# Performance work log

Measured on AMD Instinct MI355X. Metric: run time of the kernel, lower is better.

Reference implementation:

```python
import jax, jax.numpy as jnp
import numpy as np

N_HEADS = 8
N_POINTS = 4


def setup_inputs() -> dict:
    key = jax.random.key(0)
    ks = jax.random.split(key, 10)
    B, Q, D = 8, 2048, 256
    Hh, Ww = 100, 100
    s = 0.02  # init scale for weights
    return {
        "query": jax.random.normal(ks[0], (B, Q, D), jnp.float32),
        "reference_points": jax.random.uniform(ks[1], (B, Q, 2), jnp.float32),
        "input_flatten": jax.random.normal(ks[2], (B, Hh * Ww, D), jnp.float32),
        "h": Hh,
        "w": Ww,
        "W_off": jax.random.normal(ks[3], (D, N_HEADS * N_POINTS * 2), jnp.float32) * s,
        "b_off": jnp.zeros((N_HEADS * N_POINTS * 2,), jnp.float32),
        "W_attn": jax.random.normal(ks[4], (D, N_HEADS * N_POINTS), jnp.float32) * s,
        "b_attn": jnp.zeros((N_HEADS * N_POINTS,), jnp.float32),
        "W_val": jax.random.normal(ks[5], (D, D), jnp.float32) * s,
        "b_val": jnp.zeros((D,), jnp.float32),
        "W_out": jax.random.normal(ks[6], (D, D), jnp.float32) * s,
        "b_out": jnp.zeros((D,), jnp.float32),
    }


def _gather(values_heads, idx):
    # values_heads: [B, HW, H, Dh]; idx: [B, Q, H, P] -> [B, Q, H, P, Dh]
    B, HW, H, Dh = values_heads.shape
    b = jnp.arange(B)[:, None, None, None]
    hh = jnp.arange(H)[None, None, :, None]
    return values_heads[b, idx, hh, :]


def reference(query, reference_points, input_flatten, h, w,
              W_off, b_off, W_attn, b_attn, W_val, b_val, W_out, b_out):
    B, Q, D = query.shape
    HW = input_flatten.shape[1]
    nH, nP = N_HEADS, N_POINTS
    Dh = D // nH

    offsets = (query @ W_off + b_off).reshape(B, Q, nH, nP, 2)
    weights = jax.nn.softmax((query @ W_attn + b_attn).reshape(B, Q, nH, nP), axis=-1)
    values_heads = (input_flatten @ W_val + b_val).reshape(B, HW, nH, Dh)

    # sampling locations in [0,1], then to pixel coords
    loc = jnp.clip(reference_points[:, :, None, None, :] + offsets, 0.0, 1.0)
    sx = loc[..., 0] * (w - 1)  # [B,Q,H,P]
    sy = loc[..., 1] * (h - 1)

    x0 = jnp.clip(jnp.floor(sx).astype(jnp.int32), 0, w - 1)
    y0 = jnp.clip(jnp.floor(sy).astype(jnp.int32), 0, h - 1)
    x1 = jnp.clip(x0 + 1, 0, w - 1)
    y1 = jnp.clip(y0 + 1, 0, h - 1)

    wx1 = sx - x0.astype(sx.dtype)
    wx0 = 1.0 - wx1
    wy1 = sy - y0.astype(sy.dtype)
    wy0 = 1.0 - wy1

    g00 = _gather(values_heads, y0 * w + x0)
    g01 = _gather(values_heads, y1 * w + x0)
    g10 = _gather(values_heads, y0 * w + x1)
    g11 = _gather(values_heads, y1 * w + x1)

    # bilinear blend: [B,Q,H,P,Dh]
    result = (g00 * (wx0 * wy0)[..., None] + g01 * (wx0 * wy1)[..., None]
              + g10 * (wx1 * wy0)[..., None] + g11 * (wx1 * wy1)[..., None])

    out = jnp.sum(result * weights[..., None], axis=3)  # [B,Q,H,Dh]
    out = out.reshape(B, Q, D)
    return out @ W_out + b_out
```

## Files before the change

kernel.cpp:

```cpp
#include <hip/hip_runtime.h>
#include <hip/hip_bf16.h>
#include <cstdint>

#define NHEADS 8
#define NPOINTS 4

typedef __bf16 bf16x8 __attribute__((ext_vector_type(8)));
typedef float f32x4 __attribute__((ext_vector_type(4)));

#define AS1 __attribute__((address_space(1)))
#define AS3 __attribute__((address_space(3)))

__device__ __forceinline__ ushort f2bf_rn(float x) {
  union { float f; uint32_t u; } c; c.f = x;
  uint32_t r = c.u + 0x7fffu + ((c.u >> 16) & 1u);
  return (ushort)(r >> 16);
}
__device__ __forceinline__ float bf2f(ushort h) {
  union { uint32_t u; float f; } c; c.u = ((uint32_t)h) << 16; return c.f;
}
__device__ __forceinline__ uint pack2(ushort a, ushort b) {
  return (uint)a | ((uint)b << 16);
}

__device__ __forceinline__ int fr(int row) { return (row >> 1) & 3; }
__device__ __forceinline__ int aidx(int row, int gpos) { return row * 32 + gpos * 8; }

__device__ __forceinline__ int gidx8(int row, int g0) {
  return row * 64 + ((g0 ^ (row & 7)) << 3);
}

template<int TM, bool CBF16, bool ABF16>
__device__ __forceinline__ void gemm_core(
    ushort* smem, int bid,
    const void* __restrict__ Ain,
    const ushort* __restrict__ Bprep,
    const float* __restrict__ bias, void* __restrict__ Cout,
    int K)
{
  constexpr int MT = TM / 16;
  constexpr int AH = TM * 32;
  constexpr int BH = 8192;
  const int tid  = threadIdx.x;
  const int lane = tid & 63, wave = tid >> 6;
  const int wn   = wave * 64;
  const int lrow = lane & 15, lgrp = lane >> 4;
  const long brow = (long)bid * TM;
  const int NT = K >> 5;

  const float*  Af = (const float*)Ain;
  const ushort* A16 = (const ushort*)Ain;

  f32x4 acc[MT][4] = {};

  int arow, as_;
  if constexpr (TM == 64) { arow = tid >> 2; as_ = tid & 3; }
  else                    { arow = tid >> 3; as_ = tid & 7; }

  ushort* Acur = smem;
  ushort* Anxt = smem + AH;
  ushort* Bcur = smem + 2 * AH;
  ushort* Bnxt = smem + 2 * AH + BH;

#pragma unroll
  for (int i = 0; i < 4; ++i)
    __builtin_amdgcn_global_load_lds(
        (const AS1 void*)(Bprep + wave * 2048 + (lane + 64 * i) * 8),
        (AS3 void*)(Bcur + wave * 2048 + (lane + 64 * i) * 8), 16, 0, 0);
  if constexpr (ABF16) {
    uint2 av = *(const uint2*)&A16[(size_t)(brow + arow) * K + as_ * 4];
    const int g = as_ >> 1, half = (as_ & 1) * 4;
    *(uint2*)&Acur[aidx(arow, g ^ fr(arow)) + half] = av;
  } else if constexpr (TM == 64) {
    const float* ap = &Af[(size_t)(brow + arow) * K] + as_ * 8;
    float4 a0 = *(const float4*)ap, a1 = *(const float4*)(ap + 4);
    const float v[8] = {a0.x, a0.y, a0.z, a0.w, a1.x, a1.y, a1.z, a1.w};
    ushort h[8];
#pragma unroll
    for (int j = 0; j < 8; ++j) h[j] = f2bf_rn(v[j]);
    uint4 hv = {pack2(h[0],h[1]), pack2(h[2],h[3]), pack2(h[4],h[5]), pack2(h[6],h[7])};
    *(uint4*)&Acur[aidx(arow, as_ ^ fr(arow))] = hv;
  } else {
    const int g = as_ >> 1, half = (as_ & 1) * 4;
    float4 a0 = *(const float4*)&Af[(size_t)(brow + arow) * K + g * 8 + half];
    ushort h[4] = {f2bf_rn(a0.x), f2bf_rn(a0.y), f2bf_rn(a0.z), f2bf_rn(a0.w)};
    uint2 hv = {pack2(h[0],h[1]), pack2(h[2],h[3])};
    *(uint2*)&Acur[aidx(arow, g ^ fr(arow)) + half] = hv;
  }
  __syncthreads();

  for (int t = 0; t < NT; ++t) {
    const bool more = (t + 1 < NT);

    if (more) {
#pragma unroll
      for (int i = 0; i < 4; ++i)
        __builtin_amdgcn_global_load_lds(
            (const AS1 void*)(Bprep + (size_t)(t + 1) * BH + wave * 2048 + (lane + 64 * i) * 8),
            (AS3 void*)(Bnxt + wave * 2048 + (lane + 64 * i) * 8), 16, 0, 0);
    }

    float4 a0 = {}, a1 = {};
    uint2 au = {};
    if (more) {
      if constexpr (ABF16) {
        au = *(const uint2*)&A16[(size_t)(brow + arow) * K + (t + 1) * 32 + as_ * 4];
      } else if constexpr (TM == 64) {
        const float* ap = &Af[(size_t)(brow + arow) * K] + (t + 1) * 32 + as_ * 8;
        a0 = *(const float4*)ap;
        a1 = *(const float4*)(ap + 4);
      } else {
        const int g = as_ >> 1, half = (as_ & 1) * 4;
        a0 = *(const float4*)&Af[(size_t)(brow + arow) * K + (t + 1) * 32 + g * 8 + half];
      }
    }

    bf16x8 ah[MT];
#pragma unroll
    for (int mt = 0; mt < MT; ++mt) {
      const int r = mt * 16 + lrow;
      ah[mt] = *(const bf16x8*)&Acur[aidx(r, lgrp ^ fr(r))];
    }
#pragma unroll
    for (int nt = 0; nt < 4; ++nt) {
      const int r = wn + nt * 16 + lrow;
      const bf16x8 b = *(const bf16x8*)&Bcur[aidx(r, lgrp ^ fr(r))];
#pragma unroll
      for (int mt = 0; mt < MT; ++mt)
        acc[mt][nt] = __builtin_amdgcn_mfma_f32_16x16x32_bf16(ah[mt], b, acc[mt][nt], 0, 0, 0);
    }

    if (more) {
      if constexpr (ABF16) {
        const int g = as_ >> 1, half = (as_ & 1) * 4;
        *(uint2*)&Anxt[aidx(arow, g ^ fr(arow)) + half] = au;
      } else if constexpr (TM == 64) {
        const float v[8] = {a0.x, a0.y, a0.z, a0.w, a1.x, a1.y, a1.z, a1.w};
        ushort h[8];
#pragma unroll
        for (int j = 0; j < 8; ++j) h[j] = f2bf_rn(v[j]);
        uint4 hv = {pack2(h[0],h[1]), pack2(h[2],h[3]), pack2(h[4],h[5]), pack2(h[6],h[7])};
        *(uint4*)&Anxt[aidx(arow, as_ ^ fr(arow))] = hv;
      } else {
        const int g = as_ >> 1, half = (as_ & 1) * 4;
        ushort h[4] = {f2bf_rn(a0.x), f2bf_rn(a0.y), f2bf_rn(a0.z), f2bf_rn(a0.w)};
        uint2 hv = {pack2(h[0],h[1]), pack2(h[2],h[3])};
        *(uint2*)&Anxt[aidx(arow, g ^ fr(arow)) + half] = hv;
      }
    }

    __syncthreads();
    ushort* tp;
    tp = Acur; Acur = Anxt; Anxt = tp;
    tp = Bcur; Bcur = Bnxt; Bnxt = tp;
  }

  float bb[4];
#pragma unroll
  for (int nt = 0; nt < 4; ++nt) bb[nt] = bias[wn + nt * 16 + lrow];

  if constexpr (CBF16) {
    ushort* Cb = (ushort*)Cout;
    ushort* ctu = smem;
#pragma unroll
    for (int h = 0; h < TM / 32; ++h) {
      __syncthreads();
#pragma unroll
      for (int m2 = 0; m2 < 2; ++m2) {
        const int mt = h * 2 + m2;
        const int lr0 = m2 * 16 + lgrp * 4;
#pragma unroll
        for (int nt = 0; nt < 4; ++nt) {
          const int col = wn + nt * 16 + lrow;
#pragma unroll
          for (int j = 0; j < 4; ++j)
            ctu[(lr0 + j) * 264 + col] = f2bf_rn(acc[mt][nt][j] + bb[nt]);
        }
      }
      __syncthreads();
#pragma unroll
      for (int i = 0; i < 4; ++i) {
        const int idx = i * 256 + tid, r = idx >> 5, c16 = (idx & 31) * 8;
        *(uint4*)&Cb[(size_t)(brow + h * 32 + r) * 256 + c16] =
            *(const uint4*)&ctu[r * 264 + c16];
      }
    }
  } else {
    float* C = (float*)Cout;
    float* ctile = (float*)smem;
#pragma unroll
    for (int h = 0; h < MT; ++h) {
      __syncthreads();
#pragma unroll
      for (int nt = 0; nt < 4; ++nt) {
        const int col = wn + nt * 16 + lrow;
#pragma unroll
        for (int j = 0; j < 4; ++j)
          ctile[(lgrp * 4 + j) * 260 + col] = acc[h][nt][j] + bb[nt];
      }
      __syncthreads();
#pragma unroll
      for (int i = 0; i < 4; ++i) {
        const int idx = i * 256 + tid, r = idx >> 6, c4 = (idx & 63) << 2;
        *(float4*)&C[(size_t)(brow + h * 16 + r) * 256 + c4] =
            *(const float4*)&ctile[r * 260 + c4];
      }
    }
  }
}

__device__ __forceinline__ void proj_core(
    ushort* smem, int bid,
    const float* __restrict__ query,
    const ushort* __restrict__ Bprep,
    const float* __restrict__ b_off, const float* __restrict__ b_attn,
    float* __restrict__ pobuf)
{
  constexpr int AH = 32 * 64;
  constexpr int BH = 8192;
  const int tid  = threadIdx.x;
  const int lane = tid & 63, wave = tid >> 6;
  const int wm   = (wave >> 1) * 16;
  const int wn   = (wave & 1) * 64;
  const int lrow = lane & 15, lgrp = lane >> 4;
  const long brow = (long)bid * 32;

  f32x4 acc[4] = {};

  const int arow = tid >> 3, as_ = tid & 7;
  const float* Abase = &query[(size_t)(brow + arow) * 256];

  ushort* Acur = smem;
  ushort* Anxt = smem + AH;
  ushort* Bcur = smem + 2 * AH;
  ushort* Bnxt = smem + 2 * AH + BH;

#pragma unroll
  for (int i = 0; i < 4; ++i)
    __builtin_amdgcn_global_load_lds(
        (const AS1 void*)(Bprep + wave * 2048 + (lane + 64 * i) * 8),
        (AS3 void*)(Bcur + wave * 2048 + (lane + 64 * i) * 8), 16, 0, 0);
  {
    const int g = as_ >> 1, half = (as_ & 1) * 4;
    float4 a0 = *(const float4*)(Abase + g * 8 + half);
    ushort h[4], l[4];
#pragma unroll
    for (int j = 0; j < 4; ++j) {
      const float v = ((const float*)&a0)[j];
      h[j] = f2bf_rn(v);
      l[j] = f2bf_rn(v - bf2f(h[j]));
    }
    *(uint2*)&Acur[gidx8(arow, g) + half]     = uint2{pack2(h[0],h[1]), pack2(h[2],h[3])};
    *(uint2*)&Acur[gidx8(arow, g + 4) + half] = uint2{pack2(l[0],l[1]), pack2(l[2],l[3])};
  }
  __syncthreads();

  for (int t = 0; t < 8; ++t) {
    const bool more = (t + 1 < 8);

    if (more) {
#pragma unroll
      for (int i = 0; i < 4; ++i)
        __builtin_amdgcn_global_load_lds(
            (const AS1 void*)(Bprep + (size_t)(t + 1) * BH + wave * 2048 + (lane + 64 * i) * 8),
            (AS3 void*)(Bnxt + wave * 2048 + (lane + 64 * i) * 8), 16, 0, 0);
    }

    float4 a0 = {};
    const int g = as_ >> 1, half = (as_ & 1) * 4;
    if (more)
      a0 = *(const float4*)(Abase + (t + 1) * 32 + g * 8 + half);

    const int ra = wm + lrow;
    const bf16x8 ah = *(const bf16x8*)&Acur[gidx8(ra, lgrp)];
    const bf16x8 al = *(const bf16x8*)&Acur[gidx8(ra, lgrp + 4)];
#pragma unroll
    for (int nt = 0; nt < 4; ++nt) {
      const int rb = wn + nt * 16 + lrow;
      const bf16x8 bh = *(const bf16x8*)&Bcur[gidx8(rb, lgrp)];
      const bf16x8 bl = *(const bf16x8*)&Bcur[gidx8(rb, lgrp + 4)];
      acc[nt] = __builtin_amdgcn_mfma_f32_16x16x32_bf16(ah, bh, acc[nt], 0, 0, 0);
      acc[nt] = __builtin_amdgcn_mfma_f32_16x16x32_bf16(ah, bl, acc[nt], 0, 0, 0);
      acc[nt] = __builtin_amdgcn_mfma_f32_16x16x32_bf16(al, bh, acc[nt], 0, 0, 0);
    }

    if (more) {
      ushort h[4], l[4];
#pragma unroll
      for (int j = 0; j < 4; ++j) {
        const float v = ((const float*)&a0)[j];
        h[j] = f2bf_rn(v);
        l[j] = f2bf_rn(v - bf2f(h[j]));
      }
      *(uint2*)&Anxt[gidx8(arow, g) + half]     = uint2{pack2(h[0],h[1]), pack2(h[2],h[3])};
      *(uint2*)&Anxt[gidx8(arow, g + 4) + half] = uint2{pack2(l[0],l[1]), pack2(l[2],l[3])};
    }

    __syncthreads();
    ushort* tp;
    tp = Acur; Acur = Anxt; Anxt = tp;
    tp = Bcur; Bcur = Bnxt; Bnxt = tp;
  }

  __syncthreads();
  float* ctile = (float*)smem;
#pragma unroll
  for (int nt = 0; nt < 4; ++nt) {
    const int col = wn + nt * 16 + lrow;
    const float bb = (col < 64) ? b_off[col] : (col < 96 ? b_attn[col - 64] : 0.0f);
#pragma unroll
    for (int j = 0; j < 4; ++j)
      ctile[(wm + lgrp * 4 + j) * 132 + col] = acc[nt][j] + bb;
  }
  __syncthreads();
#pragma unroll
  for (int i = 0; i < 4; ++i) {
    const int idx = i * 256 + tid, r = idx >> 5, c4 = (idx & 31) * 4;
    *(float4*)&pobuf[(size_t)(brow + r) * 128 + c4] = *(const float4*)&ctile[r * 132 + c4];
  }
}

__global__ __launch_bounds__(256, 4) void fused_g1_proj(
    const float* __restrict__ input_f, const ushort* __restrict__ Bprep_val,
    const float* __restrict__ b_val, ushort* __restrict__ values,
    const float* __restrict__ query, const ushort* __restrict__ Bprep_po,
    const float* __restrict__ b_off, const float* __restrict__ b_attn,
    float* __restrict__ pobuf, int npo)
{
  __shared__ ushort smem[20480];
  const int bid = blockIdx.x;
  if (bid < npo) {
    proj_core(smem, bid, query, Bprep_po, b_off, b_attn, pobuf);
  } else {
    gemm_core<64, true, false>(smem, bid - npo, (const void*)input_f,
                               Bprep_val, b_val, (void*)values, 256);
  }
}

__global__ __launch_bounds__(256, 4) void gemm2_kernel(
    const ushort* __restrict__ midb, const ushort* __restrict__ Bprep_out,
    const float* __restrict__ b_out, float* __restrict__ out)
{
  __shared__ ushort smem[20480];
  gemm_core<32, false, true>(smem, blockIdx.x, (const void*)midb,
                             Bprep_out, b_out, (void*)out, 256);
}

__global__ __launch_bounds__(256) void prep_wt3(
    const float* __restrict__ Wv, const float* __restrict__ Wo,
    const float* __restrict__ W_off, const float* __restrict__ W_attn,
    ushort* __restrict__ Bv, ushort* __restrict__ Bo, ushort* __restrict__ Bpo)
{
  const int gid = blockIdx.x * 256 + threadIdx.x;
  if (gid < 131072) {
    const float* W = (gid < 65536) ? Wv : Wo;
    ushort* Bp     = (gid < 65536) ? Bv : Bo;
    const int pg = gid & 65535;
    const int t = pg >> 13;
    const int p = pg & 8191;
    const int r = p >> 5;
    const int q = p & 31;
    const int gpos = q >> 3;
    const int j = q & 7;
    const int g0 = gpos ^ ((r >> 1) & 3);
    const int k = t * 32 + g0 * 8 + j;
    Bp[pg] = f2bf_rn(W[(size_t)k * 256 + r]);
  } else {
    const int pg = gid - 131072;
    const int t = pg >> 13;
    const int p = pg & 8191;
    const int r = p >> 6;
    const int q = p & 63;
    const int gpos = q >> 3;
    const int j = q & 7;
    const int g0 = gpos ^ (r & 7);
    const int seg = g0 & 3, plane = g0 >> 2;
    const int k = t * 32 + seg * 8 + j;
    float w = 0.0f;
    if (r < 64)       w = W_off[(size_t)k * 64 + r];
    else if (r < 96)  w = W_attn[(size_t)k * 32 + (r - 64)];
    const ushort hi = f2bf_rn(w);
    Bpo[pg] = plane ? f2bf_rn(w - bf2f(hi)) : hi;
  }
}

__global__ __launch_bounds__(256, 8) void sample_kernel(
    const float* __restrict__ refp,
    const float* __restrict__ pobuf,
    const ushort* __restrict__ values,
    ushort* __restrict__ mid,
    const int* __restrict__ hptr, const int* __restrict__ wptr,
    int Q, int HW)
{
  const int lane = threadIdx.x & 63;
  const int cpx  = (int)gridDim.x >> 3;
  const int blk  = (blockIdx.x & 7) * cpx + (blockIdx.x >> 3);
  const int bq   = blk * 4 + (threadIdx.x >> 6);
  const int b    = bq / Q;
  const int W_   = *wptr;
  const int H_   = *hptr;
  const int h    = lane >> 3;
  const float* po = pobuf + (size_t)bq * 128;

  const float4 of0 = *(const float4*)&po[h * 8];
  const float4 of1 = *(const float4*)&po[h * 8 + 4];
  const float4 lg  = *(const float4*)&po[64 + h * 4];
  const float offx[4] = {of0.x, of0.z, of1.x, of1.z};
  const float offy[4] = {of0.y, of0.w, of1.y, of1.w};

  const float m  = fmaxf(fmaxf(lg.x, lg.y), fmaxf(lg.z, lg.w));
  const float e0 = __expf(lg.x - m), e1 = __expf(lg.y - m);
  const float e2 = __expf(lg.z - m), e3 = __expf(lg.w - m);
  const float inv = 1.0f / (e0 + e1 + e2 + e3);
  const float wt[4] = {e0 * inv, e1 * inv, e2 * inv, e3 * inv};

  const float2 rxy = *(const float2*)&refp[(size_t)bq * 2];
  const ushort* vb = values + (size_t)b * HW * 256;
  const int ch = lane * 4;

  f32x4 acc = {0.f, 0.f, 0.f, 0.f};
#pragma unroll
  for (int p = 0; p < NPOINTS; ++p) {
    float lx = rxy.x + offx[p];
    float ly = rxy.y + offy[p];
    lx = fminf(fmaxf(lx, 0.0f), 1.0f);
    ly = fminf(fmaxf(ly, 0.0f), 1.0f);
    const float sx = lx * (float)(W_ - 1);
    const float sy = ly * (float)(H_ - 1);
    int x0 = (int)floorf(sx);
    int y0 = (int)floorf(sy);
    x0 = min(max(x0, 0), W_ - 1);
    y0 = min(max(y0, 0), H_ - 1);
    const int x1 = min(x0 + 1, W_ - 1);
    const int y1 = min(y0 + 1, H_ - 1);
    const float wx1 = sx - (float)x0, wx0 = 1.0f - wx1;
    const float wy1 = sy - (float)y0, wy0 = 1.0f - wy1;

    const ushort4 g00 = *(const ushort4*)&vb[(size_t)(y0 * W_ + x0) * 256 + ch];
    const ushort4 g10 = *(const ushort4*)&vb[(size_t)(y0 * W_ + x1) * 256 + ch];
    const ushort4 g01 = *(const ushort4*)&vb[(size_t)(y1 * W_ + x0) * 256 + ch];
    const ushort4 g11 = *(const ushort4*)&vb[(size_t)(y1 * W_ + x1) * 256 + ch];

    const float w00 = wx0 * wy0, w10 = wx1 * wy0, w01 = wx0 * wy1, w11 = wx1 * wy1;
    const float wp = wt[p];
    const float f00[4] = {bf2f(g00.x), bf2f(g00.y), bf2f(g00.z), bf2f(g00.w)};
    const float f10[4] = {bf2f(g10.x), bf2f(g10.y), bf2f(g10.z), bf2f(g10.w)};
    const float f01[4] = {bf2f(g01.x), bf2f(g01.y), bf2f(g01.z), bf2f(g01.w)};
    const float f11[4] = {bf2f(g11.x), bf2f(g11.y), bf2f(g11.z), bf2f(g11.w)};
#pragma unroll
    for (int j = 0; j < 4; ++j)
      acc[j] += wp * (f00[j] * w00 + f01[j] * w01 + f10[j] * w10 + f11[j] * w11);
  }
  ushort4 mo;
  mo.x = f2bf_rn(acc[0]); mo.y = f2bf_rn(acc[1]);
  mo.z = f2bf_rn(acc[2]); mo.w = f2bf_rn(acc[3]);
  *(ushort4*)&mid[(size_t)bq * 256 + ch] = mo;
}

extern "C" void kernel_launch(void* const* d_in, const int* in_sizes, int n_in,
                              void* d_out, int out_size, void* d_ws, size_t ws_size,
                              hipStream_t stream)
{
  const float* query   = (const float*)d_in[0];
  const float* refp    = (const float*)d_in[1];
  const float* input_f = (const float*)d_in[2];
  const int*   hptr    = (const int*)d_in[3];
  const int*   wptr    = (const int*)d_in[4];
  const float* W_off   = (const float*)d_in[5];
  const float* b_off   = (const float*)d_in[6];
  const float* W_attn  = (const float*)d_in[7];
  const float* b_attn  = (const float*)d_in[8];
  const float* W_val   = (const float*)d_in[9];
  const float* b_val   = (const float*)d_in[10];
  const float* W_out   = (const float*)d_in[11];
  const float* b_out   = (const float*)d_in[12];
  float* out = (float*)d_out;

  const int D   = 256;
  const int BQ  = in_sizes[0] / D;
  const int B   = 8;
  const int Q   = BQ / B;
  const int BHW = in_sizes[2] / D;
  const int HW  = BHW / B;

  char* ws = (char*)d_ws;
  ushort* values = (ushort*)ws;
  size_t o = (size_t)BHW * D * sizeof(ushort);
  float* pobuf  = (float*)(ws + o);  o += (size_t)BQ * 128 * sizeof(float);
  ushort* midb  = (ushort*)(ws + o); o += (size_t)BQ * D * sizeof(ushort);
  ushort* Bprep_val = (ushort*)(ws + o);  o += (size_t)8 * 8192 * sizeof(ushort);
  ushort* Bprep_out = (ushort*)(ws + o);  o += (size_t)8 * 8192 * sizeof(ushort);
  ushort* Bprep_po  = (ushort*)(ws + o);  o += (size_t)8 * 8192 * sizeof(ushort);

  const int npo = BQ / 32;

  prep_wt3<<<768, 256, 0, stream>>>(W_val, W_out, W_off, W_attn,
                                    Bprep_val, Bprep_out, Bprep_po);

  fused_g1_proj<<<npo + BHW / 64, 256, 0, stream>>>(
      input_f, Bprep_val, b_val, values,
      query, Bprep_po, b_off, b_attn, pobuf, npo);

  sample_kernel<<<BQ / 4, 256, 0, stream>>>(
      refp, pobuf, values, midb, hptr, wptr, Q, HW);

  gemm2_kernel<<<BQ / 32, 256, 0, stream>>>(
      midb, Bprep_out, b_out, out);
}
```

Baseline: 63.04 us.

## Fuse bilinear sampling into output projection GEMM via LDS-resident tile

Merges the sampling kernel and the output-projection GEMM into one kernel. Each block samples 32 queries, with one thread per (query, head) accumulating 32 channels, and writes the bf16 result straight into LDS. It then runs an MFMA GEMM against double-buffered weight tiles loaded with global_load_lds. This removes the intermediate midb round-trip through global memory and one kernel launch. In exchange there are far fewer threads doing the gathers (512 blocks of 256), more registers per thread, and lower occupancy, so gather latency may be poorly hidden.

```diff
diff --git a/kernel.cpp b/kernel.cpp
--- a/kernel.cpp
+++ b/kernel.cpp
@@ -337,13 +337,168 @@
   }
 }
 
-__global__ __launch_bounds__(256, 4) void gemm2_kernel(
-    const ushort* __restrict__ midb, const ushort* __restrict__ Bprep_out,
-    const float* __restrict__ b_out, float* __restrict__ out)
+__global__ __launch_bounds__(256, 3) void sample_gemm2(
+    const float* __restrict__ refp,
+    const float* __restrict__ pobuf,
+    const ushort* __restrict__ values,
+    const ushort* __restrict__ Bprep,
+    const float* __restrict__ b_out, float* __restrict__ out,
+    const int* __restrict__ hptr, const int* __restrict__ wptr,
+    int Q, int HW)
 {
-  __shared__ ushort smem[20480];
-  gemm_core<32, false, true>(smem, blockIdx.x, (const void*)midb,
-                             Bprep_out, b_out, (void*)out, 256);
+  constexpr int BH = 8192;
+  __shared__ ushort smem[8192 + 2 * BH];
+  ushort* Amid = smem;
+  ushort* Bcur = smem + 8192;
+  ushort* Bnxt = smem + 8192 + BH;
+
+  const int tid  = threadIdx.x;
+  const int lane = tid & 63, wave = tid >> 6;
+  const int s    = ((int)blockIdx.x & 7) * ((int)gridDim.x >> 3) + ((int)blockIdx.x >> 3);
+  const long brow = (long)s * 32;
+
+#pragma unroll
+  for (int i = 0; i < 4; ++i)
+    __builtin_amdgcn_global_load_lds(
+        (const AS1 void*)(Bprep + wave * 2048 + (lane + 64 * i) * 8),
+        (AS3 void*)(Bcur + wave * 2048 + (lane + 64 * i) * 8), 16, 0, 0);
+
+  {
+    const int q_l = tid >> 3, h = tid & 7;
+    const long gq = brow + q_l;
+    const int b = (int)(gq / Q);
+    const int W_ = *wptr, H_ = *hptr;
+    const float* po = pobuf + gq * 128;
+
+    const float4 of0 = *(const float4*)&po[h * 8];
+    const float4 of1 = *(const float4*)&po[h * 8 + 4];
+    const float4 lg  = *(const float4*)&po[64 + h * 4];
+    const float offx[4] = {of0.x, of0.z, of1.x, of1.z};
+    const float offy[4] = {of0.y, of0.w, of1.y, of1.w};
+
+    const float m  = fmaxf(fmaxf(lg.x, lg.y), fmaxf(lg.z, lg.w));
+    const float e0 = __expf(lg.x - m), e1 = __expf(lg.y - m);
+    const float e2 = __expf(lg.z - m), e3 = __expf(lg.w - m);
+    const float inv = 1.0f / (e0 + e1 + e2 + e3);
+    const float wt[4] = {e0 * inv, e1 * inv, e2 * inv, e3 * inv};
+
+    const float2 rxy = *(const float2*)&refp[gq * 2];
+    const ushort* vb = values + (size_t)b * HW * 256 + h * 32;
+
+    float acc1[32] = {};
+#pragma unroll
+    for (int p = 0; p < NPOINTS; ++p) {
+      float lx = rxy.x + offx[p];
+      float ly = rxy.y + offy[p];
+      lx = fminf(fmaxf(lx, 0.0f), 1.0f);
+      ly = fminf(fmaxf(ly, 0.0f), 1.0f);
+      const float sx = lx * (float)(W_ - 1);
+      const float sy = ly * (float)(H_ - 1);
+      int x0 = (int)floorf(sx);
+      int y0 = (int)floorf(sy);
+      x0 = min(max(x0, 0), W_ - 1);
+      y0 = min(max(y0, 0), H_ - 1);
+      const int x1 = min(x0 + 1, W_ - 1);
+      const int y1 = min(y0 + 1, H_ - 1);
+      const float wx1 = sx - (float)x0, wx0 = 1.0f - wx1;
+      const float wy1 = sy - (float)y0, wy0 = 1.0f - wy1;
+      const float w00 = wx0 * wy0, w10 = wx1 * wy0, w01 = wx0 * wy1, w11 = wx1 * wy1;
+      const float wp = wt[p];
+
+      const ushort* c00 = &vb[(size_t)(y0 * W_ + x0) * 256];
+      const ushort* c10 = &vb[(size_t)(y0 * W_ + x1) * 256];
+      const ushort* c01 = &vb[(size_t)(y1 * W_ + x0) * 256];
+      const ushort* c11 = &vb[(size_t)(y1 * W_ + x1) * 256];
+#pragma unroll
+      for (int g = 0; g < 4; ++g) {
+        const ushort4 v00a = *(const ushort4*)(c00 + g * 8);
+        const ushort4 v00b = *(const ushort4*)(c00 + g * 8 + 4);
+        const ushort4 v10a = *(const ushort4*)(c10 + g * 8);
+        const ushort4 v10b = *(const ushort4*)(c10 + g * 8 + 4);
+        const ushort4 v01a = *(const ushort4*)(c01 + g * 8);
+        const ushort4 v01b = *(const ushort4*)(c01 + g * 8 + 4);
+        const ushort4 v11a = *(const ushort4*)(c11 + g * 8);
+        const ushort4 v11b = *(const ushort4*)(c11 + g * 8 + 4);
+        const ushort u00[8] = {v00a.x,v00a.y,v00a.z,v00a.w,v00b.x,v00b.y,v00b.z,v00b.w};
+        const ushort u10[8] = {v10a.x,v10a.y,v10a.z,v10a.w,v10b.x,v10b.y,v10b.z,v10b.w};
+        const ushort u01[8] = {v01a.x,v01a.y,v01a.z,v01a.w,v01b.x,v01b.y,v01b.z,v01b.w};
+        const ushort u11[8] = {v11a.x,v11a.y,v11a.z,v11a.w,v11b.x,v11b.y,v11b.z,v11b.w};
+#pragma unroll
+        for (int j = 0; j < 8; ++j)
+          acc1[g * 8 + j] += wp * (bf2f(u00[j]) * w00 + bf2f(u01[j]) * w01 +
+                                   bf2f(u10[j]) * w10 + bf2f(u11[j]) * w11);
+      }
+    }
+
+#pragma unroll
+    for (int g = 0; g < 4; ++g) {
+      ushort hh[8];
+#pragma unroll
+      for (int j = 0; j < 8; ++j) hh[j] = f2bf_rn(acc1[g * 8 + j]);
+      uint4 hv = {pack2(hh[0],hh[1]), pack2(hh[2],hh[3]),
+                  pack2(hh[4],hh[5]), pack2(hh[6],hh[7])};
+      *(uint4*)&Amid[h * 1024 + aidx(q_l, g ^ fr(q_l))] = hv;
+    }
+  }
+  __syncthreads();
+
+  {
+    const int wn   = wave * 64;
+    const int lrow = lane & 15, lgrp = lane >> 4;
+    f32x4 acc[2][4] = {};
+
+    for (int t = 0; t < 8; ++t) {
+      const bool more = (t + 1 < 8);
+      if (more) {
+#pragma unroll
+        for (int i = 0; i < 4; ++i)
+          __builtin_amdgcn_global_load_lds(
+              (const AS1 void*)(Bprep + (size_t)(t + 1) * BH + wave * 2048 + (lane + 64 * i) * 8),
+              (AS3 void*)(Bnxt + wave * 2048 + (lane + 64 * i) * 8), 16, 0, 0);
+      }
+
+      bf16x8 ah[2];
+#pragma unroll
+      for (int mt = 0; mt < 2; ++mt) {
+        const int r = mt * 16 + lrow;
+        ah[mt] = *(const bf16x8*)&Amid[t * 1024 + aidx(r, lgrp ^ fr(r))];
+      }
+#pragma unroll
+      for (int nt = 0; nt < 4; ++nt) {
+        const int r = wn + nt * 16 + lrow;
+        const bf16x8 b = *(const bf16x8*)&Bcur[aidx(r, lgrp ^ fr(r))];
+#pragma unroll
+        for (int mt = 0; mt < 2; ++mt)
+          acc[mt][nt] = __builtin_amdgcn_mfma_f32_16x16x32_bf16(ah[mt], b, acc[mt][nt], 0, 0, 0);
+      }
+
+      __syncthreads();
+      ushort* tp = Bcur; Bcur = Bnxt; Bnxt = tp;
+    }
+
+    float bb[4];
+#pragma unroll
+    for (int nt = 0; nt < 4; ++nt) bb[nt] = b_out[wn + nt * 16 + lrow];
+    float* ctile = (float*)smem;
+#pragma unroll
+    for (int h = 0; h < 2; ++h) {
+      __syncthreads();
+#pragma unroll
+      for (int nt = 0; nt < 4; ++nt) {
+        const int col = wn + nt * 16 + lrow;
+#pragma unroll
+        for (int j = 0; j < 4; ++j)
+          ctile[(lgrp * 4 + j) * 260 + col] = acc[h][nt][j] + bb[nt];
+      }
+      __syncthreads();
+#pragma unroll
+      for (int i = 0; i < 4; ++i) {
+        const int idx = i * 256 + tid, r = idx >> 6, c4 = (idx & 63) << 2;
+        *(float4*)&out[(size_t)(brow + h * 16 + r) * 256 + c4] =
+            *(const float4*)&ctile[r * 260 + c4];
+      }
+    }
+  }
 }
 
 __global__ __launch_bounds__(256) void prep_wt3(
@@ -384,79 +539,6 @@
   }
 }
 
-__global__ __launch_bounds__(256, 8) void sample_kernel(
-    const float* __restrict__ refp,
-    const float* __restrict__ pobuf,
-    const ushort* __restrict__ values,
-    ushort* __restrict__ mid,
-    const int* __restrict__ hptr, const int* __restrict__ wptr,
-    int Q, int HW)
-{
-  const int lane = threadIdx.x & 63;
-  const int cpx  = (int)gridDim.x >> 3;
-  const int blk  = (blockIdx.x & 7) * cpx + (blockIdx.x >> 3);
-  const int bq   = blk * 4 + (threadIdx.x >> 6);
-  const int b    = bq / Q;
-  const int W_   = *wptr;
-  const int H_   = *hptr;
-  const int h    = lane >> 3;
-  const float* po = pobuf + (size_t)bq * 128;
-
-  const float4 of0 = *(const float4*)&po[h * 8];
-  const float4 of1 = *(const float4*)&po[h * 8 + 4];
-  const float4 lg  = *(const float4*)&po[64 + h * 4];
-  const float offx[4] = {of0.x, of0.z, of1.x, of1.z};
-  const float offy[4] = {of0.y, of0.w, of1.y, of1.w};
-
-  const float m  = fmaxf(fmaxf(lg.x, lg.y), fmaxf(lg.z, lg.w));
-  const float e0 = __expf(lg.x - m), e1 = __expf(lg.y - m);
-  const float e2 = __expf(lg.z - m), e3 = __expf(lg.w - m);
-  const float inv = 1.0f / (e0 + e1 + e2 + e3);
-  const float wt[4] = {e0 * inv, e1 * inv, e2 * inv, e3 * inv};
-
-  const float2 rxy = *(const float2*)&refp[(size_t)bq * 2];
-  const ushort* vb = values + (size_t)b * HW * 256;
-  const int ch = lane * 4;
-
-  f32x4 acc = {0.f, 0.f, 0.f, 0.f};
-#pragma unroll
-  for (int p = 0; p < NPOINTS; ++p) {
-    float lx = rxy.x + offx[p];
-    float ly = rxy.y + offy[p];
-    lx = fminf(fmaxf(lx, 0.0f), 1.0f);
-    ly = fminf(fmaxf(ly, 0.0f), 1.0f);
-    const float sx = lx * (float)(W_ - 1);
-    const float sy = ly * (float)(H_ - 1);
-    int x0 = (int)floorf(sx);
-    int y0 = (int)floorf(sy);
-    x0 = min(max(x0, 0), W_ - 1);
-    y0 = min(max(y0, 0), H_ - 1);
-    const int x1 = min(x0 + 1, W_ - 1);
-    const int y1 = min(y0 + 1, H_ - 1);
-    const float wx1 = sx - (float)x0, wx0 = 1.0f - wx1;
-    const float wy1 = sy - (float)y0, wy0 = 1.0f - wy1;
-
-    const ushort4 g00 = *(const ushort4*)&vb[(size_t)(y0 * W_ + x0) * 256 + ch];
-    const ushort4 g10 = *(const ushort4*)&vb[(size_t)(y0 * W_ + x1) * 256 + ch];
-    const ushort4 g01 = *(const ushort4*)&vb[(size_t)(y1 * W_ + x0) * 256 + ch];
-    const ushort4 g11 = *(const ushort4*)&vb[(size_t)(y1 * W_ + x1) * 256 + ch];
-
-    const float w00 = wx0 * wy0, w10 = wx1 * wy0, w01 = wx0 * wy1, w11 = wx1 * wy1;
-    const float wp = wt[p];
-    const float f00[4] = {bf2f(g00.x), bf2f(g00.y), bf2f(g00.z), bf2f(g00.w)};
-    const float f10[4] = {bf2f(g10.x), bf2f(g10.y), bf2f(g10.z), bf2f(g10.w)};
-    const float f01[4] = {bf2f(g01.x), bf2f(g01.y), bf2f(g01.z), bf2f(g01.w)};
-    const float f11[4] = {bf2f(g11.x), bf2f(g11.y), bf2f(g11.z), bf2f(g11.w)};
-#pragma unroll
-    for (int j = 0; j < 4; ++j)
-      acc[j] += wp * (f00[j] * w00 + f01[j] * w01 + f10[j] * w10 + f11[j] * w11);
-  }
-  ushort4 mo;
-  mo.x = f2bf_rn(acc[0]); mo.y = f2bf_rn(acc[1]);
-  mo.z = f2bf_rn(acc[2]); mo.w = f2bf_rn(acc[3]);
-  *(ushort4*)&mid[(size_t)bq * 256 + ch] = mo;
-}
-
 extern "C" void kernel_launch(void* const* d_in, const int* in_sizes, int n_in,
                               void* d_out, int out_size, void* d_ws, size_t ws_size,
                               hipStream_t stream)
@@ -487,7 +569,6 @@
   ushort* values = (ushort*)ws;
   size_t o = (size_t)BHW * D * sizeof(ushort);
   float* pobuf  = (float*)(ws + o);  o += (size_t)BQ * 128 * sizeof(float);
-  ushort* midb  = (ushort*)(ws + o); o += (size_t)BQ * D * sizeof(ushort);
   ushort* Bprep_val = (ushort*)(ws + o);  o += (size_t)8 * 8192 * sizeof(ushort);
   ushort* Bprep_out = (ushort*)(ws + o);  o += (size_t)8 * 8192 * sizeof(ushort);
   ushort* Bprep_po  = (ushort*)(ws + o);  o += (size_t)8 * 8192 * sizeof(ushort);
@@ -501,9 +582,6 @@
       input_f, Bprep_val, b_val, values,
       query, Bprep_po, b_off, b_attn, pobuf, npo);
 
-  sample_kernel<<<BQ / 4, 256, 0, stream>>>(
-      refp, pobuf, values, midb, hptr, wptr, Q, HW);
-
-  gemm2_kernel<<<BQ / 32, 256, 0, stream>>>(
-      midb, Bprep_out, b_out, out);
-}
+  sample_gemm2<<<BQ / 32, 256, 0, stream>>>(
+      refp, pobuf, values, Bprep_out, b_out, out, hptr, wptr, Q, HW);
+}
```

After: 96.97 us. 53.8% more time.
